# Optimization experiments

Hardware: AMD Instinct MI355X
Metric: run time of the kernel (lower is better)

## Reference

```python
import jax, jax.numpy as jnp
import numpy as np

N = 8192      # num voxels (queries)
M = 8192      # num important conv coords (keys)
B = 2         # batch size
MAXZ, MAXY, MAXX = 41, 1440, 1440
PTS, PDIM = 5, 4
PRUNE_RATIO = 0.5
NEG = -1e9


def setup_inputs() -> dict:
    key = jax.random.key(0)
    k = jax.random.split(key, 8)
    bidx = jax.random.randint(k[0], (N, 1), 0, B)
    zyx = jnp.concatenate([
        jax.random.randint(k[1], (N, 1), 0, MAXZ),
        jax.random.randint(k[2], (N, 1), 0, MAXY),
        jax.random.randint(k[3], (N, 1), 0, MAXX)], axis=1)
    voxel_coords = jnp.concatenate([bidx, zyx], axis=1).astype(jnp.int32)  # [N,4] (b,z,y,x)
    kb = jax.random.randint(k[4], (M, 1), 0, B).astype(jnp.float32)
    kc = jax.random.uniform(k[5], (M, 3), dtype=jnp.float32) * jnp.array([MAXZ, MAXY, MAXX], jnp.float32)
    important_conv_coords = jnp.concatenate([kb, kc], axis=1)  # [M,4] float
    voxels = jax.random.normal(k[6], (N, PTS, PDIM), dtype=jnp.float32)
    kw = jax.random.split(k[7], 2)
    w1 = jax.random.normal(kw[0], (3, 32), dtype=jnp.float32) * 0.5
    b1 = jnp.zeros((32,), jnp.float32)
    w2 = jax.random.normal(kw[1], (32, 1), dtype=jnp.float32) * 0.2
    b2 = jnp.zeros((1,), jnp.float32)
    return {"voxel_coords": voxel_coords, "important_conv_coords": important_conv_coords,
            "voxels": voxels, "w1": w1, "b1": b1, "w2": w2, "b2": b2}


def reference(voxel_coords, important_conv_coords, voxels, w1, b1, w2, b2):
    # --- attn_prune_unimportant: per-batch coord attention, vectorized with a batch mask ---
    q = voxel_coords[:, 1:].astype(jnp.float32)           # [N,3]
    qb = voxel_coords[:, 0]                               # [N] batch idx
    keys = important_conv_coords[:, 1:]                   # [M,3]
    kbat = important_conv_coords[:, 0].astype(jnp.int32)  # [M]
    scores = jnp.einsum('nd,md->nm', q, keys) / jnp.sqrt(jnp.float32(3.0))  # [N,M]
    mask = qb[:, None] == kbat[None, :]
    scores = jnp.where(mask, scores, NEG)
    attn = jax.nn.softmax(scores, axis=-1)                # per-batch softmax (masked)
    coords_weight = jnp.einsum('nm,md->nd', attn, keys)   # [N,3]  (values == keys)
    # importance_conv: Linear(3,32) -> ReLU -> Linear(32,1) -> Sigmoid
    h = jax.nn.relu(coords_weight @ w1 + b1)
    importance = jax.nn.sigmoid(h @ w2 + b2)              # [N,1]
    # --- sort-based pruning: drop the lowest-importance fraction ---
    order = jnp.argsort(importance[:, 0])                 # ascending, like torch .sort()
    keep = order[int(N * PRUNE_RATIO):]                   # [K] static size
    important_coords = voxel_coords[keep]                 # [K,4]
    important_voxels = voxels[keep]                       # [K,PTS,PDIM]
    kept_importance = importance[keep]                    # [K,1]
    return important_coords, important_voxels, kept_importance, importance
```

## Files before the change

kernel.cpp:

```cpp
#include <hip/hip_runtime.h>
#include <math.h>

#define NQ   8192
#define MK   8192
#define KEEP 4096

#define OFF_HDR    0
#define OFF_KPART  64
#define OFF_QPART  131136
#define OFF_CMAX   262208
#define OFF_PART   524352
#define OFF_K64    1572928


typedef unsigned long long ull;

__global__ __launch_bounds__(1024) void partition_kernel(
    const int4*   __restrict__ vcoords,
    const float4* __restrict__ kcoords,
    float* __restrict__ ws)
{
    __shared__ int wtot[16];
    const int t = threadIdx.x, w = t >> 6, lane = t & 63;
    const int base = t * 8;
    int* hdr = (int*)ws;
    float4* kp = (float4*)((char*)ws + OFF_KPART);
    float4* qp = (float4*)((char*)ws + OFF_QPART);

    float4 kv[8];
    int n0 = 0;
    #pragma unroll
    for (int r = 0; r < 8; ++r) { kv[r] = kcoords[base + r]; n0 += (kv[r].x == 0.0f) ? 1 : 0; }
    int inc = n0;
    #pragma unroll
    for (int off = 1; off < 64; off <<= 1) { int a = __shfl_up(inc, off); if (lane >= off) inc += a; }
    if (lane == 63) wtot[w] = inc;
    __syncthreads();
    int wbase = 0, tot0 = 0;
    #pragma unroll
    for (int i = 0; i < 16; ++i) { if (i < w) wbase += wtot[i]; tot0 += wtot[i]; }
    int ex0 = wbase + inc - n0;
    int ex1 = tot0 + (base - ex0);
    #pragma unroll
    for (int r = 0; r < 8; ++r) {
        if (kv[r].x == 0.0f) kp[ex0++] = kv[r]; else kp[ex1++] = kv[r];
    }
    if (t == 0) { hdr[0] = tot0; hdr[1] = MK - tot0; }
    __syncthreads();

    int4 qv[8];
    int qn0 = 0;
    #pragma unroll
    for (int r = 0; r < 8; ++r) { qv[r] = vcoords[base + r]; qn0 += (qv[r].x == 0) ? 1 : 0; }
    int qinc = qn0;
    #pragma unroll
    for (int off = 1; off < 64; off <<= 1) { int a = __shfl_up(qinc, off); if (lane >= off) qinc += a; }
    if (lane == 63) wtot[w] = qinc;
    __syncthreads();
    int qwbase = 0, qtot0 = 0;
    #pragma unroll
    for (int i = 0; i < 16; ++i) { if (i < w) qwbase += wtot[i]; qtot0 += wtot[i]; }
    int qex0 = qwbase + qinc - qn0;
    int qex1 = qtot0 + (base - qex0);
    #pragma unroll
    for (int r = 0; r < 8; ++r) {
        int idx = base + r;
        float4 q;
        q.x = (float)qv[r].y; q.y = (float)qv[r].z; q.z = (float)qv[r].w;
        q.w = __int_as_float(idx);
        if (qv[r].x == 0) qp[qex0++] = q; else qp[qex1++] = q;
    }
    if (t == 0) { hdr[2] = qtot0; hdr[3] = NQ - qtot0; }
}

__global__ __launch_bounds__(1024) void attn_kernel(float* __restrict__ ws)
{
    __shared__ __align__(16) char smem[65792];
    float4* sk   = (float4*)smem;
    float*  red1 = (float*)(smem + 16384);
    float*  red2 = (float*)(smem + 16384 + 16448);
    float4* pf   = (float4*)smem;

    const int* hdr = (const int*)ws;
    const float4* kpart = (const float4*)((char*)ws + OFF_KPART);
    const float4* qpart = (const float4*)((char*)ws + OFF_QPART);
    float*  cmaxg = (float*)((char*)ws + OFF_CMAX);
    float4* partg = (float4*)((char*)ws + OFF_PART);

    const int kc0 = hdr[0], qc0 = hdr[2];
    const int g = blockIdx.x >> 3, c = blockIdx.x & 7;
    const int gs = g * 256;
    const bool uni1 = (gs >= qc0);
    const bool uni  = (gs + 256 <= qc0) || uni1;
    const int r0  = (uni && uni1) ? kc0 : 0;
    const int len = uni ? (uni1 ? MK - kc0 : kc0) : MK;
    const int CL = (len + 7) >> 3;
    const int cs = r0 + c * CL;
    int tn = min(cs + CL, r0 + len) - cs; if (tn < 0) tn = 0;

    const int t = threadIdx.x, w = t >> 6, lane = t & 63;
    const float4 q0 = qpart[gs + lane];
    const float4 q1 = qpart[gs + lane + 64];
    const float4 q2 = qpart[gs + lane + 128];
    const float4 q3 = qpart[gs + lane + 192];
    const float b0 = (gs + lane        >= qc0) ? 1.f : 0.f;
    const float b1 = (gs + lane + 64   >= qc0) ? 1.f : 0.f;
    const float b2_ = (gs + lane + 128 >= qc0) ? 1.f : 0.f;
    const float b3 = (gs + lane + 192  >= qc0) ? 1.f : 0.f;
    const float is3 = 0.57735026918962576f;

    if (t < tn) sk[t] = kpart[cs + t];
    __syncthreads();

    const int SL = (tn + 15) >> 4;
    const int jb = w * SL, je = min(jb + SL, tn);

    float m0 = -INFINITY, m1 = -INFINITY, m2 = -INFINITY, m3 = -INFINITY;
    if (uni) {
        #pragma unroll 4
        for (int j = jb; j < je; ++j) {
            float4 k4 = sk[j];
            m0 = fmaxf(m0, fmaf(q0.x, k4.y, fmaf(q0.y, k4.z, q0.z * k4.w)));
            m1 = fmaxf(m1, fmaf(q1.x, k4.y, fmaf(q1.y, k4.z, q1.z * k4.w)));
            m2 = fmaxf(m2, fmaf(q2.x, k4.y, fmaf(q2.y, k4.z, q2.z * k4.w)));
            m3 = fmaxf(m3, fmaf(q3.x, k4.y, fmaf(q3.y, k4.z, q3.z * k4.w)));
        }
    } else {
        #pragma unroll 4
        for (int j = jb; j < je; ++j) {
            float4 k4 = sk[j];
            float d0 = fmaf(q0.x, k4.y, fmaf(q0.y, k4.z, q0.z * k4.w));
            float d1 = fmaf(q1.x, k4.y, fmaf(q1.y, k4.z, q1.z * k4.w));
            float d2 = fmaf(q2.x, k4.y, fmaf(q2.y, k4.z, q2.z * k4.w));
            float d3 = fmaf(q3.x, k4.y, fmaf(q3.y, k4.z, q3.z * k4.w));
            m0 = fmaxf(m0, fmaf(fabsf(k4.x - b0),  -1e10f, d0));
            m1 = fmaxf(m1, fmaf(fabsf(k4.x - b1),  -1e10f, d1));
            m2 = fmaxf(m2, fmaf(fabsf(k4.x - b2_), -1e10f, d2));
            m3 = fmaxf(m3, fmaf(fabsf(k4.x - b3),  -1e10f, d3));
        }
    }
    red1[w * 257 + lane]       = m0;
    red1[w * 257 + lane + 64]  = m1;
    red1[w * 257 + lane + 128] = m2;
    red1[w * 257 + lane + 192] = m3;
    __syncthreads();
    {
        const int col = t >> 2, r4 = (t & 3) * 4;
        float mv = red1[r4 * 257 + col];
        mv = fmaxf(mv, red1[(r4 + 1) * 257 + col]);
        mv = fmaxf(mv, red1[(r4 + 2) * 257 + col]);
        mv = fmaxf(mv, red1[(r4 + 3) * 257 + col]);
        mv = fmaxf(mv, __shfl_xor(mv, 1));
        mv = fmaxf(mv, __shfl_xor(mv, 2));
        if ((t & 3) == 0) {
            red2[col] = mv;
            cmaxg[blockIdx.x * 256 + col] = mv;
        }
    }
    __syncthreads();
    const float mg0 = red2[lane],       cut0 = mg0 - 155.8845727f;
    const float mg1 = red2[lane + 64],  cut1 = mg1 - 155.8845727f;
    const float mg2 = red2[lane + 128], cut2 = mg2 - 155.8845727f;
    const float mg3 = red2[lane + 192], cut3 = mg3 - 155.8845727f;

    float l0 = 0.f, sz0 = 0.f, sy0 = 0.f, sx0 = 0.f;
    float l1 = 0.f, sz1 = 0.f, sy1 = 0.f, sx1 = 0.f;
    float l2 = 0.f, sz2 = 0.f, sy2 = 0.f, sx2 = 0.f;
    float l3 = 0.f, sz3 = 0.f, sy3 = 0.f, sx3 = 0.f;
    #pragma unroll 2
    for (int j = jb; j < je; ++j) {
        float4 k4 = sk[j];
        float d0 = fmaf(q0.x, k4.y, fmaf(q0.y, k4.z, q0.z * k4.w));
        float d1 = fmaf(q1.x, k4.y, fmaf(q1.y, k4.z, q1.z * k4.w));
        float d2 = fmaf(q2.x, k4.y, fmaf(q2.y, k4.z, q2.z * k4.w));
        float d3 = fmaf(q3.x, k4.y, fmaf(q3.y, k4.z, q3.z * k4.w));
        if (!uni) {
            d0 = fmaf(fabsf(k4.x - b0),  -1e10f, d0);
            d1 = fmaf(fabsf(k4.x - b1),  -1e10f, d1);
            d2 = fmaf(fabsf(k4.x - b2_), -1e10f, d2);
            d3 = fmaf(fabsf(k4.x - b3),  -1e10f, d3);
        }
        bool t0 = d0 >= cut0, t1 = d1 >= cut1, t2 = d2 >= cut2, t3 = d3 >= cut3;
        if (__any(t0 || t1 || t2 || t3)) {
            float e0 = t0 ? expf((d0 - mg0) * is3) : 0.f;
            float e1 = t1 ? expf((d1 - mg1) * is3) : 0.f;
            float e2 = t2 ? expf((d2 - mg2) * is3) : 0.f;
            float e3 = t3 ? expf((d3 - mg3) * is3) : 0.f;
            l0 += e0; sz0 = fmaf(e0, k4.y, sz0); sy0 = fmaf(e0, k4.z, sy0); sx0 = fmaf(e0, k4.w, sx0);
            l1 += e1; sz1 = fmaf(e1, k4.y, sz1); sy1 = fmaf(e1, k4.z, sy1); sx1 = fmaf(e1, k4.w, sx1);
            l2 += e2; sz2 = fmaf(e2, k4.y, sz2); sy2 = fmaf(e2, k4.z, sy2); sx2 = fmaf(e2, k4.w, sx2);
            l3 += e3; sz3 = fmaf(e3, k4.y, sz3); sy3 = fmaf(e3, k4.z, sy3); sx3 = fmaf(e3, k4.w, sx3);
        }
    }
    __syncthreads();
    pf[w * 257 + lane]       = make_float4(l0, sz0, sy0, sx0);
    pf[w * 257 + lane + 64]  = make_float4(l1, sz1, sy1, sx1);
    pf[w * 257 + lane + 128] = make_float4(l2, sz2, sy2, sx2);
    pf[w * 257 + lane + 192] = make_float4(l3, sz3, sy3, sx3);
    __syncthreads();
    {
        const int col = t >> 2, r4 = (t & 3) * 4;
        float4 a = pf[r4 * 257 + col];
        #pragma unroll
        for (int rr = 1; rr < 4; ++rr) {
            float4 p = pf[(r4 + rr) * 257 + col];
            a.x += p.x; a.y += p.y; a.z += p.z; a.w += p.w;
        }
        a.x += __shfl_xor(a.x, 1); a.y += __shfl_xor(a.y, 1);
        a.z += __shfl_xor(a.z, 1); a.w += __shfl_xor(a.w, 1);
        a.x += __shfl_xor(a.x, 2); a.y += __shfl_xor(a.y, 2);
        a.z += __shfl_xor(a.z, 2); a.w += __shfl_xor(a.w, 2);
        if ((t & 3) == 0) partg[blockIdx.x * 256 + col] = a;
    }
}

__global__ __launch_bounds__(256) void mlp_kernel(
    const float* __restrict__ ws,
    const float* __restrict__ w1, const float* __restrict__ b1,
    const float* __restrict__ w2, const float* __restrict__ b2,
    float* __restrict__ out_imp, ull* __restrict__ K64)
{
    const int s = blockIdx.x * 256 + threadIdx.x;
    const int g = s >> 8, q = s & 255;
    const float*  cmaxg = (const float*)((const char*)ws + OFF_CMAX);
    const float4* partg = (const float4*)((const char*)ws + OFF_PART);
    const float4* qpart = (const float4*)((const char*)ws + OFF_QPART);
    const float is3 = 0.57735026918962576f;

    float cc[8];
    float C = -INFINITY;
    #pragma unroll
    for (int c = 0; c < 8; ++c) {
        cc[c] = cmaxg[(g * 8 + c) * 256 + q];
        C = fmaxf(C, cc[c]);
    }
    float L = 0.f, SZ = 0.f, SY = 0.f, SX = 0.f;
    if (C != -INFINITY) {
        #pragma unroll
        for (int c = 0; c < 8; ++c) {
            float sc = expf((cc[c] - C) * is3);
            float4 p = partg[(g * 8 + c) * 256 + q];
            L  = fmaf(p.x, sc, L);
            SZ = fmaf(p.y, sc, SZ);
            SY = fmaf(p.z, sc, SY);
            SX = fmaf(p.w, sc, SX);
        }
    }
    const float4 qq = qpart[s];
    const int qid = __float_as_int(qq.w);
    float inv = (L > 0.f) ? 1.f / L : 0.f;
    float cz = SZ * inv, cy = SY * inv, cx = SX * inv;
    float logit = b2[0];
    #pragma unroll
    for (int k = 0; k < 32; ++k) {
        float h = b1[k] + cz * w1[k] + cy * w1[32 + k] + cx * w1[64 + k];
        h = fmaxf(h, 0.f);
        logit += h * w2[k];
    }
    float p = 1.f / (1.f + expf(-logit));
    out_imp[qid] = p;
    K64[qid] = ((ull)__float_as_uint(p) << 32) | (unsigned)qid;
}

__global__ __launch_bounds__(1024) void rank_scatter_kernel(
    const ull* __restrict__ K,
    const int4* __restrict__ vcoords,
    const float* __restrict__ voxels,
    float* __restrict__ out)
{
    __shared__ int scnt[16][32];
    __shared__ int rks[32];
    const int t = threadIdx.x, w = t >> 6, lane = t & 63;
    const int ib = blockIdx.x * 32;

    const ull kiv = K[ib + (lane & 31)];
    const int kilo = (int)(unsigned)kiv, kihi = (int)(unsigned)(kiv >> 32);

    const int jb = w * 512;
    ull kj[8];
    #pragma unroll
    for (int r = 0; r < 8; ++r) kj[r] = K[jb + r * 64 + lane];

    int acc = 0;
    for (int i = 0; i < 32; ++i) {
        unsigned lo = (unsigned)__builtin_amdgcn_readlane(kilo, i);
        unsigned hi = (unsigned)__builtin_amdgcn_readlane(kihi, i);
        ull ki = ((ull)hi << 32) | lo;
        int c = 0;
        #pragma unroll
        for (int r = 0; r < 8; ++r)
            c += (int)__popcll(__ballot(kj[r] < ki));
        acc += (lane == i) ? c : 0;
    }
    if (lane < 32) scnt[w][lane] = acc;
    __syncthreads();
    if (t < 32) {
        int rank = 0;
        #pragma unroll
        for (int ww = 0; ww < 16; ++ww) rank += scnt[ww][t];
        rks[t] = rank;
    }
    __syncthreads();

    const int il = t >> 5, r = t & 31;
    const int rank = rks[il];
    if (rank >= KEEP) {
        const int p = rank - KEEP;
        const int i = ib + il;
        if (r < 20) {
            out[16384 + p * 20 + r] = voxels[i * 20 + r];
        } else if (r < 24) {
            const int* vc = (const int*)&vcoords[i];
            out[p * 4 + (r - 20)] = (float)vc[r - 20];
        } else if (r == 24) {
            out[98304 + p] = __uint_as_float((unsigned)(K[i] >> 32));
        }
    }
}

extern "C" void kernel_launch(void* const* d_in, const int* in_sizes, int n_in,
                              void* d_out, int out_size, void* d_ws, size_t ws_size,
                              hipStream_t stream) {
    const int4*   vcoords = (const int4*)d_in[0];
    const float4* kcoords = (const float4*)d_in[1];
    const float*  voxels  = (const float*)d_in[2];
    const float*  w1      = (const float*)d_in[3];
    const float*  b1      = (const float*)d_in[4];
    const float*  w2      = (const float*)d_in[5];
    const float*  b2      = (const float*)d_in[6];
    float* out = (float*)d_out;
    float* ws  = (float*)d_ws;
    ull* K64   = (ull*)((char*)d_ws + OFF_K64);

    partition_kernel<<<1, 1024, 0, stream>>>(vcoords, kcoords, ws);
    attn_kernel<<<256, 1024, 0, stream>>>(ws);
    mlp_kernel<<<32, 256, 0, stream>>>(ws, w1, b1, w2, b2, out + 102400, K64);
    rank_scatter_kernel<<<256, 1024, 0, stream>>>(K64, vcoords, voxels, out);
}
```

Before: 118.9 us.

## Fuse four kernels into one persistent kernel with grid-wide atomic barriers

Merges the partition, attention, MLP and rank/scatter kernels into a single 256-block launch, with hand-written atomic grid barriers separating the phases. The single-block partition becomes a parallel per-block count, then a scan over the block counts and a scatter. This removes three kernel launch gaps and the serial one-block partition stage. In exchange it adds four grid syncs and a memset to clear the barrier counters, and it depends on all 256 blocks of 1024 threads being resident at once or it will deadlock.

```diff
diff --git a/kernel.cpp b/kernel.cpp
--- a/kernel.cpp
+++ b/kernel.cpp
@@ -4,316 +4,331 @@
 #define NQ   8192
 #define MK   8192
 #define KEEP 4096
-
-#define OFF_HDR    0
-#define OFF_KPART  64
-#define OFF_QPART  131136
-#define OFF_CMAX   262208
-#define OFF_PART   524352
-#define OFF_K64    1572928
+#define NBLK 256
+
+#define OFF_BAR    0
+#define OFF_KCNT   64
+#define OFF_QCNT   1088
+#define OFF_KPART  2112
+#define OFF_QPART  133184
+#define OFF_CMAX   264256
+#define OFF_PART   526400
+#define OFF_K64    1574976
 
 
 typedef unsigned long long ull;
 
-__global__ __launch_bounds__(1024) void partition_kernel(
+__device__ __forceinline__ void grid_barrier(unsigned* bar, int ph) {
+    __syncthreads();
+    if (threadIdx.x == 0) {
+        __threadfence();
+        unsigned prev = atomicAdd(bar + ph * 2, 1u);
+        if (prev == NBLK - 1u) {
+            atomicExch(bar + ph * 2 + 1, 1u);
+        } else {
+            while (atomicAdd(bar + ph * 2 + 1, 0u) == 0u)
+                __builtin_amdgcn_s_sleep(2);
+        }
+        __threadfence();
+    }
+    __syncthreads();
+}
+
+__global__ __launch_bounds__(1024) void fused_kernel(
     const int4*   __restrict__ vcoords,
     const float4* __restrict__ kcoords,
-    float* __restrict__ ws)
-{
-    __shared__ int wtot[16];
-    const int t = threadIdx.x, w = t >> 6, lane = t & 63;
-    const int base = t * 8;
-    int* hdr = (int*)ws;
-    float4* kp = (float4*)((char*)ws + OFF_KPART);
-    float4* qp = (float4*)((char*)ws + OFF_QPART);
-
-    float4 kv[8];
-    int n0 = 0;
-    #pragma unroll
-    for (int r = 0; r < 8; ++r) { kv[r] = kcoords[base + r]; n0 += (kv[r].x == 0.0f) ? 1 : 0; }
-    int inc = n0;
-    #pragma unroll
-    for (int off = 1; off < 64; off <<= 1) { int a = __shfl_up(inc, off); if (lane >= off) inc += a; }
-    if (lane == 63) wtot[w] = inc;
-    __syncthreads();
-    int wbase = 0, tot0 = 0;
-    #pragma unroll
-    for (int i = 0; i < 16; ++i) { if (i < w) wbase += wtot[i]; tot0 += wtot[i]; }
-    int ex0 = wbase + inc - n0;
-    int ex1 = tot0 + (base - ex0);
-    #pragma unroll
-    for (int r = 0; r < 8; ++r) {
-        if (kv[r].x == 0.0f) kp[ex0++] = kv[r]; else kp[ex1++] = kv[r];
-    }
-    if (t == 0) { hdr[0] = tot0; hdr[1] = MK - tot0; }
-    __syncthreads();
-
-    int4 qv[8];
-    int qn0 = 0;
-    #pragma unroll
-    for (int r = 0; r < 8; ++r) { qv[r] = vcoords[base + r]; qn0 += (qv[r].x == 0) ? 1 : 0; }
-    int qinc = qn0;
-    #pragma unroll
-    for (int off = 1; off < 64; off <<= 1) { int a = __shfl_up(qinc, off); if (lane >= off) qinc += a; }
-    if (lane == 63) wtot[w] = qinc;
-    __syncthreads();
-    int qwbase = 0, qtot0 = 0;
-    #pragma unroll
-    for (int i = 0; i < 16; ++i) { if (i < w) qwbase += wtot[i]; qtot0 += wtot[i]; }
-    int qex0 = qwbase + qinc - qn0;
-    int qex1 = qtot0 + (base - qex0);
-    #pragma unroll
-    for (int r = 0; r < 8; ++r) {
-        int idx = base + r;
-        float4 q;
-        q.x = (float)qv[r].y; q.y = (float)qv[r].z; q.z = (float)qv[r].w;
-        q.w = __int_as_float(idx);
-        if (qv[r].x == 0) qp[qex0++] = q; else qp[qex1++] = q;
-    }
-    if (t == 0) { hdr[2] = qtot0; hdr[3] = NQ - qtot0; }
-}
-
-__global__ __launch_bounds__(1024) void attn_kernel(float* __restrict__ ws)
+    const float*  __restrict__ voxels,
+    const float*  __restrict__ w1, const float* __restrict__ b1v,
+    const float*  __restrict__ w2, const float* __restrict__ b2v,
+    float* __restrict__ out,
+    void*  __restrict__ wsv)
 {
     __shared__ __align__(16) char smem[65792];
-    float4* sk   = (float4*)smem;
-    float*  red1 = (float*)(smem + 16384);
-    float*  red2 = (float*)(smem + 16384 + 16448);
-    float4* pf   = (float4*)smem;
-
-    const int* hdr = (const int*)ws;
-    const float4* kpart = (const float4*)((char*)ws + OFF_KPART);
-    const float4* qpart = (const float4*)((char*)ws + OFF_QPART);
-    float*  cmaxg = (float*)((char*)ws + OFF_CMAX);
-    float4* partg = (float4*)((char*)ws + OFF_PART);
-
-    const int kc0 = hdr[0], qc0 = hdr[2];
-    const int g = blockIdx.x >> 3, c = blockIdx.x & 7;
-    const int gs = g * 256;
-    const bool uni1 = (gs >= qc0);
-    const bool uni  = (gs + 256 <= qc0) || uni1;
-    const int r0  = (uni && uni1) ? kc0 : 0;
-    const int len = uni ? (uni1 ? MK - kc0 : kc0) : MK;
-    const int CL = (len + 7) >> 3;
-    const int cs = r0 + c * CL;
-    int tn = min(cs + CL, r0 + len) - cs; if (tn < 0) tn = 0;
-
-    const int t = threadIdx.x, w = t >> 6, lane = t & 63;
-    const float4 q0 = qpart[gs + lane];
-    const float4 q1 = qpart[gs + lane + 64];
-    const float4 q2 = qpart[gs + lane + 128];
-    const float4 q3 = qpart[gs + lane + 192];
-    const float b0 = (gs + lane        >= qc0) ? 1.f : 0.f;
-    const float b1 = (gs + lane + 64   >= qc0) ? 1.f : 0.f;
-    const float b2_ = (gs + lane + 128 >= qc0) ? 1.f : 0.f;
-    const float b3 = (gs + lane + 192  >= qc0) ? 1.f : 0.f;
-    const float is3 = 0.57735026918962576f;
-
-    if (t < tn) sk[t] = kpart[cs + t];
+    __shared__ int shdr[4];
+    __shared__ int scnt[16][32];
+    __shared__ int rks[32];
+
+    unsigned* bar  = (unsigned*)((char*)wsv + OFF_BAR);
+    unsigned* kcnt = (unsigned*)((char*)wsv + OFF_KCNT);
+    unsigned* qcnt = (unsigned*)((char*)wsv + OFF_QCNT);
+    float4*   kpart = (float4*)((char*)wsv + OFF_KPART);
+    float4*   qpart = (float4*)((char*)wsv + OFF_QPART);
+    float*    cmaxg = (float*)((char*)wsv + OFF_CMAX);
+    float4*   partg = (float4*)((char*)wsv + OFF_PART);
+    ull*      K64   = (ull*)((char*)wsv + OFF_K64);
+
+    const int b = blockIdx.x, t = threadIdx.x;
+    const int w = t >> 6, lane = t & 63;
+
+    float4 myK = make_float4(0,0,0,0);
+    int4   myQ = make_int4(0,0,0,0);
+    ull blK = 0, blQ = 0;
+    if (w == 0) {
+        if (lane < 32) myK = kcoords[b * 32 + lane];
+        blK = __ballot((lane < 32) && (myK.x == 0.0f));
+        if (lane == 0) kcnt[b] = (unsigned)__popcll(blK);
+    } else if (w == 1) {
+        if (lane < 32) myQ = vcoords[b * 32 + lane];
+        blQ = __ballot((lane < 32) && (myQ.x == 0));
+        if (lane == 0) qcnt[b] = (unsigned)__popcll(blQ);
+    }
+    grid_barrier(bar, 0);
+
+    if (w < 2) {
+        const unsigned* cnt = (w == 0) ? kcnt : qcnt;
+        unsigned c0 = cnt[4*lane], c1 = cnt[4*lane+1],
+                 c2 = cnt[4*lane+2], c3 = cnt[4*lane+3];
+        unsigned s = c0 + c1 + c2 + c3;
+        unsigned sc = s;
+        #pragma unroll
+        for (int off = 1; off < 64; off <<= 1) {
+            unsigned v = __shfl_up(sc, off);
+            if (lane >= off) sc += v;
+        }
+        unsigned tot  = __shfl(sc, 63);
+        unsigned excl = sc - s;
+        const int lb = b >> 2, rb = b & 3;
+        unsigned p = (rb == 0) ? 0u : (rb == 1) ? c0 :
+                     (rb == 2) ? (c0 + c1) : (c0 + c1 + c2);
+        unsigned base = (unsigned)__shfl((int)excl, lb) + (unsigned)__shfl((int)p, lb);
+        if (lane == 0) { shdr[w * 2] = (int)base; shdr[w * 2 + 1] = (int)tot; }
+    }
     __syncthreads();
-
-    const int SL = (tn + 15) >> 4;
-    const int jb = w * SL, je = min(jb + SL, tn);
-
-    float m0 = -INFINITY, m1 = -INFINITY, m2 = -INFINITY, m3 = -INFINITY;
-    if (uni) {
-        #pragma unroll 4
-        for (int j = jb; j < je; ++j) {
-            float4 k4 = sk[j];
-            m0 = fmaxf(m0, fmaf(q0.x, k4.y, fmaf(q0.y, k4.z, q0.z * k4.w)));
-            m1 = fmaxf(m1, fmaf(q1.x, k4.y, fmaf(q1.y, k4.z, q1.z * k4.w)));
-            m2 = fmaxf(m2, fmaf(q2.x, k4.y, fmaf(q2.y, k4.z, q2.z * k4.w)));
-            m3 = fmaxf(m3, fmaf(q3.x, k4.y, fmaf(q3.y, k4.z, q3.z * k4.w)));
-        }
-    } else {
-        #pragma unroll 4
+    const int kOff = shdr[0], kc0 = shdr[1];
+    const int qOff = shdr[2], qc0 = shdr[3];
+
+    if (w == 0 && lane < 32) {
+        bool p0 = (myK.x == 0.0f);
+        int bef = (int)__popcll(blK & ((1ull << lane) - 1));
+        int gi = b * 32 + lane;
+        int dst = p0 ? (kOff + bef) : (kc0 + gi - (kOff + bef));
+        kpart[dst] = myK;
+    } else if (w == 1 && lane < 32) {
+        bool p0 = (myQ.x == 0);
+        int bef = (int)__popcll(blQ & ((1ull << lane) - 1));
+        int gi = b * 32 + lane;
+        int dst = p0 ? (qOff + bef) : (qc0 + gi - (qOff + bef));
+        qpart[dst] = make_float4((float)myQ.y, (float)myQ.z, (float)myQ.w,
+                                 __int_as_float(gi));
+    }
+    grid_barrier(bar, 1);
+
+    {
+        float4* sk   = (float4*)smem;
+        float*  red1 = (float*)(smem + 16384);
+        float*  red2 = (float*)(smem + 16384 + 16448);
+        float4* pf   = (float4*)smem;
+
+        const int g = b >> 3, c = b & 7;
+        const int gs = g * 256;
+        const bool uni1 = (gs >= qc0);
+        const bool uni  = (gs + 256 <= qc0) || uni1;
+        const int r0  = (uni && uni1) ? kc0 : 0;
+        const int len = uni ? (uni1 ? MK - kc0 : kc0) : MK;
+        const int CL = (len + 7) >> 3;
+        const int cs = r0 + c * CL;
+        int tn = min(cs + CL, r0 + len) - cs; if (tn < 0) tn = 0;
+
+        const float4 q0 = qpart[gs + lane];
+        const float4 q1 = qpart[gs + lane + 64];
+        const float4 q2 = qpart[gs + lane + 128];
+        const float4 q3 = qpart[gs + lane + 192];
+        const float f0 = (gs + lane       >= qc0) ? 1.f : 0.f;
+        const float f1 = (gs + lane + 64  >= qc0) ? 1.f : 0.f;
+        const float f2 = (gs + lane + 128 >= qc0) ? 1.f : 0.f;
+        const float f3 = (gs + lane + 192 >= qc0) ? 1.f : 0.f;
+        const float is3 = 0.57735026918962576f;
+
+        if (t < tn) sk[t] = kpart[cs + t];
+        __syncthreads();
+
+        const int SL = (tn + 15) >> 4;
+        const int jb = w * SL, je = min(jb + SL, tn);
+
+        float m0 = -INFINITY, m1 = -INFINITY, m2 = -INFINITY, m3 = -INFINITY;
+        if (uni) {
+            #pragma unroll 4
+            for (int j = jb; j < je; ++j) {
+                float4 k4 = sk[j];
+                m0 = fmaxf(m0, fmaf(q0.x, k4.y, fmaf(q0.y, k4.z, q0.z * k4.w)));
+                m1 = fmaxf(m1, fmaf(q1.x, k4.y, fmaf(q1.y, k4.z, q1.z * k4.w)));
+                m2 = fmaxf(m2, fmaf(q2.x, k4.y, fmaf(q2.y, k4.z, q2.z * k4.w)));
+                m3 = fmaxf(m3, fmaf(q3.x, k4.y, fmaf(q3.y, k4.z, q3.z * k4.w)));
+            }
+        } else {
+            #pragma unroll 4
+            for (int j = jb; j < je; ++j) {
+                float4 k4 = sk[j];
+                float d0 = fmaf(q0.x, k4.y, fmaf(q0.y, k4.z, q0.z * k4.w));
+                float d1 = fmaf(q1.x, k4.y, fmaf(q1.y, k4.z, q1.z * k4.w));
+                float d2 = fmaf(q2.x, k4.y, fmaf(q2.y, k4.z, q2.z * k4.w));
+                float d3 = fmaf(q3.x, k4.y, fmaf(q3.y, k4.z, q3.z * k4.w));
+                m0 = fmaxf(m0, fmaf(fabsf(k4.x - f0), -1e10f, d0));
+                m1 = fmaxf(m1, fmaf(fabsf(k4.x - f1), -1e10f, d1));
+                m2 = fmaxf(m2, fmaf(fabsf(k4.x - f2), -1e10f, d2));
+                m3 = fmaxf(m3, fmaf(fabsf(k4.x - f3), -1e10f, d3));
+            }
+        }
+        red1[w * 257 + lane]       = m0;
+        red1[w * 257 + lane + 64]  = m1;
+        red1[w * 257 + lane + 128] = m2;
+        red1[w * 257 + lane + 192] = m3;
+        __syncthreads();
+        {
+            const int col = t >> 2, r4 = (t & 3) * 4;
+            float mv = red1[r4 * 257 + col];
+            mv = fmaxf(mv, red1[(r4 + 1) * 257 + col]);
+            mv = fmaxf(mv, red1[(r4 + 2) * 257 + col]);
+            mv = fmaxf(mv, red1[(r4 + 3) * 257 + col]);
+            mv = fmaxf(mv, __shfl_xor(mv, 1));
+            mv = fmaxf(mv, __shfl_xor(mv, 2));
+            if ((t & 3) == 0) {
+                red2[col] = mv;
+                cmaxg[b * 256 + col] = mv;
+            }
+        }
+        __syncthreads();
+        const float mg0 = red2[lane],       cut0 = mg0 - 155.8845727f;
+        const float mg1 = red2[lane + 64],  cut1 = mg1 - 155.8845727f;
+        const float mg2 = red2[lane + 128], cut2 = mg2 - 155.8845727f;
+        const float mg3 = red2[lane + 192], cut3 = mg3 - 155.8845727f;
+
+        float l0 = 0.f, sz0 = 0.f, sy0 = 0.f, sx0 = 0.f;
+        float l1 = 0.f, sz1 = 0.f, sy1 = 0.f, sx1 = 0.f;
+        float l2 = 0.f, sz2 = 0.f, sy2 = 0.f, sx2 = 0.f;
+        float l3 = 0.f, sz3 = 0.f, sy3 = 0.f, sx3 = 0.f;
+        #pragma unroll 2
         for (int j = jb; j < je; ++j) {
             float4 k4 = sk[j];
             float d0 = fmaf(q0.x, k4.y, fmaf(q0.y, k4.z, q0.z * k4.w));
             float d1 = fmaf(q1.x, k4.y, fmaf(q1.y, k4.z, q1.z * k4.w));
             float d2 = fmaf(q2.x, k4.y, fmaf(q2.y, k4.z, q2.z * k4.w));
             float d3 = fmaf(q3.x, k4.y, fmaf(q3.y, k4.z, q3.z * k4.w));
-            m0 = fmaxf(m0, fmaf(fabsf(k4.x - b0),  -1e10f, d0));
-            m1 = fmaxf(m1, fmaf(fabsf(k4.x - b1),  -1e10f, d1));
-            m2 = fmaxf(m2, fmaf(fabsf(k4.x - b2_), -1e10f, d2));
-            m3 = fmaxf(m3, fmaf(fabsf(k4.x - b3),  -1e10f, d3));
-        }
-    }
-    red1[w * 257 + lane]       = m0;
-    red1[w * 257 + lane + 64]  = m1;
-    red1[w * 257 + lane + 128] = m2;
-    red1[w * 257 + lane + 192] = m3;
-    __syncthreads();
-    {
-        const int col = t >> 2, r4 = (t & 3) * 4;
-        float mv = red1[r4 * 257 + col];
-        mv = fmaxf(mv, red1[(r4 + 1) * 257 + col]);
-        mv = fmaxf(mv, red1[(r4 + 2) * 257 + col]);
-        mv = fmaxf(mv, red1[(r4 + 3) * 257 + col]);
-        mv = fmaxf(mv, __shfl_xor(mv, 1));
-        mv = fmaxf(mv, __shfl_xor(mv, 2));
-        if ((t & 3) == 0) {
-            red2[col] = mv;
-            cmaxg[blockIdx.x * 256 + col] = mv;
-        }
-    }
-    __syncthreads();
-    const float mg0 = red2[lane],       cut0 = mg0 - 155.8845727f;
-    const float mg1 = red2[lane + 64],  cut1 = mg1 - 155.8845727f;
-    const float mg2 = red2[lane + 128], cut2 = mg2 - 155.8845727f;
-    const float mg3 = red2[lane + 192], cut3 = mg3 - 155.8845727f;
-
-    float l0 = 0.f, sz0 = 0.f, sy0 = 0.f, sx0 = 0.f;
-    float l1 = 0.f, sz1 = 0.f, sy1 = 0.f, sx1 = 0.f;
-    float l2 = 0.f, sz2 = 0.f, sy2 = 0.f, sx2 = 0.f;
-    float l3 = 0.f, sz3 = 0.f, sy3 = 0.f, sx3 = 0.f;
-    #pragma unroll 2
-    for (int j = jb; j < je; ++j) {
-        float4 k4 = sk[j];
-        float d0 = fmaf(q0.x, k4.y, fmaf(q0.y, k4.z, q0.z * k4.w));
-        float d1 = fmaf(q1.x, k4.y, fmaf(q1.y, k4.z, q1.z * k4.w));
-        float d2 = fmaf(q2.x, k4.y, fmaf(q2.y, k4.z, q2.z * k4.w));
-        float d3 = fmaf(q3.x, k4.y, fmaf(q3.y, k4.z, q3.z * k4.w));
-        if (!uni) {
-            d0 = fmaf(fabsf(k4.x - b0),  -1e10f, d0);
-            d1 = fmaf(fabsf(k4.x - b1),  -1e10f, d1);
-            d2 = fmaf(fabsf(k4.x - b2_), -1e10f, d2);
-            d3 = fmaf(fabsf(k4.x - b3),  -1e10f, d3);
-        }
-        bool t0 = d0 >= cut0, t1 = d1 >= cut1, t2 = d2 >= cut2, t3 = d3 >= cut3;
-        if (__any(t0 || t1 || t2 || t3)) {
-            float e0 = t0 ? expf((d0 - mg0) * is3) : 0.f;
-            float e1 = t1 ? expf((d1 - mg1) * is3) : 0.f;
-            float e2 = t2 ? expf((d2 - mg2) * is3) : 0.f;
-            float e3 = t3 ? expf((d3 - mg3) * is3) : 0.f;
-            l0 += e0; sz0 = fmaf(e0, k4.y, sz0); sy0 = fmaf(e0, k4.z, sy0); sx0 = fmaf(e0, k4.w, sx0);
-            l1 += e1; sz1 = fmaf(e1, k4.y, sz1); sy1 = fmaf(e1, k4.z, sy1); sx1 = fmaf(e1, k4.w, sx1);
-            l2 += e2; sz2 = fmaf(e2, k4.y, sz2); sy2 = fmaf(e2, k4.z, sy2); sx2 = fmaf(e2, k4.w, sx2);
-            l3 += e3; sz3 = fmaf(e3, k4.y, sz3); sy3 = fmaf(e3, k4.z, sy3); sx3 = fmaf(e3, k4.w, sx3);
-        }
-    }
-    __syncthreads();
-    pf[w * 257 + lane]       = make_float4(l0, sz0, sy0, sx0);
-    pf[w * 257 + lane + 64]  = make_float4(l1, sz1, sy1, sx1);
-    pf[w * 257 + lane + 128] = make_float4(l2, sz2, sy2, sx2);
-    pf[w * 257 + lane + 192] = make_float4(l3, sz3, sy3, sx3);
-    __syncthreads();
-    {
-        const int col = t >> 2, r4 = (t & 3) * 4;
-        float4 a = pf[r4 * 257 + col];
-        #pragma unroll
-        for (int rr = 1; rr < 4; ++rr) {
-            float4 p = pf[(r4 + rr) * 257 + col];
-            a.x += p.x; a.y += p.y; a.z += p.z; a.w += p.w;
-        }
-        a.x += __shfl_xor(a.x, 1); a.y += __shfl_xor(a.y, 1);
-        a.z += __shfl_xor(a.z, 1); a.w += __shfl_xor(a.w, 1);
-        a.x += __shfl_xor(a.x, 2); a.y += __shfl_xor(a.y, 2);
-        a.z += __shfl_xor(a.z, 2); a.w += __shfl_xor(a.w, 2);
-        if ((t & 3) == 0) partg[blockIdx.x * 256 + col] = a;
-    }
-}
-
-__global__ __launch_bounds__(256) void mlp_kernel(
-    const float* __restrict__ ws,
-    const float* __restrict__ w1, const float* __restrict__ b1,
-    const float* __restrict__ w2, const float* __restrict__ b2,
-    float* __restrict__ out_imp, ull* __restrict__ K64)
-{
-    const int s = blockIdx.x * 256 + threadIdx.x;
-    const int g = s >> 8, q = s & 255;
-    const float*  cmaxg = (const float*)((const char*)ws + OFF_CMAX);
-    const float4* partg = (const float4*)((const char*)ws + OFF_PART);
-    const float4* qpart = (const float4*)((const char*)ws + OFF_QPART);
-    const float is3 = 0.57735026918962576f;
-
-    float cc[8];
-    float C = -INFINITY;
-    #pragma unroll
-    for (int c = 0; c < 8; ++c) {
-        cc[c] = cmaxg[(g * 8 + c) * 256 + q];
-        C = fmaxf(C, cc[c]);
-    }
-    float L = 0.f, SZ = 0.f, SY = 0.f, SX = 0.f;
-    if (C != -INFINITY) {
+            if (!uni) {
+                d0 = fmaf(fabsf(k4.x - f0), -1e10f, d0);
+                d1 = fmaf(fabsf(k4.x - f1), -1e10f, d1);
+                d2 = fmaf(fabsf(k4.x - f2), -1e10f, d2);
+                d3 = fmaf(fabsf(k4.x - f3), -1e10f, d3);
+            }
+            bool t0 = d0 >= cut0, t1 = d1 >= cut1, t2 = d2 >= cut2, t3 = d3 >= cut3;
+            if (__any(t0 || t1 || t2 || t3)) {
+                float e0 = t0 ? expf((d0 - mg0) * is3) : 0.f;
+                float e1 = t1 ? expf((d1 - mg1) * is3) : 0.f;
+                float e2 = t2 ? expf((d2 - mg2) * is3) : 0.f;
+                float e3 = t3 ? expf((d3 - mg3) * is3) : 0.f;
+                l0 += e0; sz0 = fmaf(e0, k4.y, sz0); sy0 = fmaf(e0, k4.z, sy0); sx0 = fmaf(e0, k4.w, sx0);
+                l1 += e1; sz1 = fmaf(e1, k4.y, sz1); sy1 = fmaf(e1, k4.z, sy1); sx1 = fmaf(e1, k4.w, sx1);
+                l2 += e2; sz2 = fmaf(e2, k4.y, sz2); sy2 = fmaf(e2, k4.z, sy2); sx2 = fmaf(e2, k4.w, sx2);
+                l3 += e3; sz3 = fmaf(e3, k4.y, sz3); sy3 = fmaf(e3, k4.z, sy3); sx3 = fmaf(e3, k4.w, sx3);
+            }
+        }
+        __syncthreads();
+        pf[w * 257 + lane]       = make_float4(l0, sz0, sy0, sx0);
+        pf[w * 257 + lane + 64]  = make_float4(l1, sz1, sy1, sx1);
+        pf[w * 257 + lane + 128] = make_float4(l2, sz2, sy2, sx2);
+        pf[w * 257 + lane + 192] = make_float4(l3, sz3, sy3, sx3);
+        __syncthreads();
+        {
+            const int col = t >> 2, r4 = (t & 3) * 4;
+            float4 a = pf[r4 * 257 + col];
+            #pragma unroll
+            for (int rr = 1; rr < 4; ++rr) {
+                float4 p = pf[(r4 + rr) * 257 + col];
+                a.x += p.x; a.y += p.y; a.z += p.z; a.w += p.w;
+            }
+            a.x += __shfl_xor(a.x, 1); a.y += __shfl_xor(a.y, 1);
+            a.z += __shfl_xor(a.z, 1); a.w += __shfl_xor(a.w, 1);
+            a.x += __shfl_xor(a.x, 2); a.y += __shfl_xor(a.y, 2);
+            a.z += __shfl_xor(a.z, 2); a.w += __shfl_xor(a.w, 2);
+            if ((t & 3) == 0) partg[b * 256 + col] = a;
+        }
+    }
+    grid_barrier(bar, 2);
+
+    if (t < 32) {
+        const int s = b * 32 + t;
+        const int g = s >> 8, q = s & 255;
+        const float is3 = 0.57735026918962576f;
+        float cc[8];
+        float C = -INFINITY;
         #pragma unroll
         for (int c = 0; c < 8; ++c) {
-            float sc = expf((cc[c] - C) * is3);
-            float4 p = partg[(g * 8 + c) * 256 + q];
-            L  = fmaf(p.x, sc, L);
-            SZ = fmaf(p.y, sc, SZ);
-            SY = fmaf(p.z, sc, SY);
-            SX = fmaf(p.w, sc, SX);
-        }
-    }
-    const float4 qq = qpart[s];
-    const int qid = __float_as_int(qq.w);
-    float inv = (L > 0.f) ? 1.f / L : 0.f;
-    float cz = SZ * inv, cy = SY * inv, cx = SX * inv;
-    float logit = b2[0];
-    #pragma unroll
-    for (int k = 0; k < 32; ++k) {
-        float h = b1[k] + cz * w1[k] + cy * w1[32 + k] + cx * w1[64 + k];
-        h = fmaxf(h, 0.f);
-        logit += h * w2[k];
-    }
-    float p = 1.f / (1.f + expf(-logit));
-    out_imp[qid] = p;
-    K64[qid] = ((ull)__float_as_uint(p) << 32) | (unsigned)qid;
-}
-
-__global__ __launch_bounds__(1024) void rank_scatter_kernel(
-    const ull* __restrict__ K,
-    const int4* __restrict__ vcoords,
-    const float* __restrict__ voxels,
-    float* __restrict__ out)
-{
-    __shared__ int scnt[16][32];
-    __shared__ int rks[32];
-    const int t = threadIdx.x, w = t >> 6, lane = t & 63;
-    const int ib = blockIdx.x * 32;
-
-    const ull kiv = K[ib + (lane & 31)];
-    const int kilo = (int)(unsigned)kiv, kihi = (int)(unsigned)(kiv >> 32);
-
-    const int jb = w * 512;
-    ull kj[8];
-    #pragma unroll
-    for (int r = 0; r < 8; ++r) kj[r] = K[jb + r * 64 + lane];
-
-    int acc = 0;
-    for (int i = 0; i < 32; ++i) {
-        unsigned lo = (unsigned)__builtin_amdgcn_readlane(kilo, i);
-        unsigned hi = (unsigned)__builtin_amdgcn_readlane(kihi, i);
-        ull ki = ((ull)hi << 32) | lo;
-        int c = 0;
+            cc[c] = cmaxg[(g * 8 + c) * 256 + q];
+            C = fmaxf(C, cc[c]);
+        }
+        float L = 0.f, SZ = 0.f, SY = 0.f, SX = 0.f;
+        if (C != -INFINITY) {
+            #pragma unroll
+            for (int c = 0; c < 8; ++c) {
+                float scale = expf((cc[c] - C) * is3);
+                float4 p = partg[(g * 8 + c) * 256 + q];
+                L  = fmaf(p.x, scale, L);
+                SZ = fmaf(p.y, scale, SZ);
+                SY = fmaf(p.z, scale, SY);
+                SX = fmaf(p.w, scale, SX);
+            }
+        }
+        const float4 qq = qpart[s];
+        const int qid = __float_as_int(qq.w);
+        float inv = (L > 0.f) ? 1.f / L : 0.f;
+        float cz = SZ * inv, cy = SY * inv, cx = SX * inv;
+        float logit = b2v[0];
         #pragma unroll
-        for (int r = 0; r < 8; ++r)
-            c += (int)__popcll(__ballot(kj[r] < ki));
-        acc += (lane == i) ? c : 0;
-    }
-    if (lane < 32) scnt[w][lane] = acc;
-    __syncthreads();
-    if (t < 32) {
-        int rank = 0;
+        for (int k = 0; k < 32; ++k) {
+            float h = b1v[k] + cz * w1[k] + cy * w1[32 + k] + cx * w1[64 + k];
+            h = fmaxf(h, 0.f);
+            logit += h * w2[k];
+        }
+        float p = 1.f / (1.f + expf(-logit));
+        out[102400 + qid] = p;
+        K64[qid] = ((ull)__float_as_uint(p) << 32) | (unsigned)qid;
+    }
+    grid_barrier(bar, 3);
+
+    {
+        const int ib = b * 32;
+        const ull kiv = K64[ib + (lane & 31)];
+        const int kilo = (int)(unsigned)kiv, kihi = (int)(unsigned)(kiv >> 32);
+
+        const int jb = w * 512;
+        ull kj[8];
         #pragma unroll
-        for (int ww = 0; ww < 16; ++ww) rank += scnt[ww][t];
-        rks[t] = rank;
-    }
-    __syncthreads();
-
-    const int il = t >> 5, r = t & 31;
-    const int rank = rks[il];
-    if (rank >= KEEP) {
-        const int p = rank - KEEP;
-        const int i = ib + il;
-        if (r < 20) {
-            out[16384 + p * 20 + r] = voxels[i * 20 + r];
-        } else if (r < 24) {
-            const int* vc = (const int*)&vcoords[i];
-            out[p * 4 + (r - 20)] = (float)vc[r - 20];
-        } else if (r == 24) {
-            out[98304 + p] = __uint_as_float((unsigned)(K[i] >> 32));
+        for (int r = 0; r < 8; ++r) kj[r] = K64[jb + r * 64 + lane];
+
+        int acc = 0;
+        for (int i = 0; i < 32; ++i) {
+            unsigned lo = (unsigned)__builtin_amdgcn_readlane(kilo, i);
+            unsigned hi = (unsigned)__builtin_amdgcn_readlane(kihi, i);
+            ull ki = ((ull)hi << 32) | lo;
+            int c = 0;
+            #pragma unroll
+            for (int r = 0; r < 8; ++r)
+                c += (int)__popcll(__ballot(kj[r] < ki));
+            acc += (lane == i) ? c : 0;
+        }
+        if (lane < 32) scnt[w][lane] = acc;
+        __syncthreads();
+        if (t < 32) {
+            int rank = 0;
+            #pragma unroll
+            for (int ww = 0; ww < 16; ++ww) rank += scnt[ww][t];
+            rks[t] = rank;
+        }
+        __syncthreads();
+
+        const int il = t >> 5, r = t & 31;
+        const int rank = rks[il];
+        if (rank >= KEEP) {
+            const int p = rank - KEEP;
+            const int i = ib + il;
+            if (r < 20) {
+                out[16384 + p * 20 + r] = voxels[i * 20 + r];
+            } else if (r < 24) {
+                const int* vc = (const int*)&vcoords[i];
+                out[p * 4 + (r - 20)] = (float)vc[r - 20];
+            } else if (r == 24) {
+                out[98304 + p] = __uint_as_float((unsigned)(K64[i] >> 32));
+            }
         }
     }
 }
@@ -329,11 +344,8 @@
     const float*  w2      = (const float*)d_in[5];
     const float*  b2      = (const float*)d_in[6];
     float* out = (float*)d_out;
-    float* ws  = (float*)d_ws;
-    ull* K64   = (ull*)((char*)d_ws + OFF_K64);
-
-    partition_kernel<<<1, 1024, 0, stream>>>(vcoords, kcoords, ws);
-    attn_kernel<<<256, 1024, 0, stream>>>(ws);
-    mlp_kernel<<<32, 256, 0, stream>>>(ws, w1, b1, w2, b2, out + 102400, K64);
-    rank_scatter_kernel<<<256, 1024, 0, stream>>>(K64, vcoords, voxels, out);
+
+    hipMemsetAsync(d_ws, 0, 64, stream);
+    fused_kernel<<<NBLK, 1024, 0, stream>>>(vcoords, kcoords, voxels,
+                                            w1, b1, w2, b2, out, d_ws);
 }
```

Measured after the change: 148.0 us. +24.4%, slower.

## Drop batch partition kernel and apply masked attention over all keys

Applied to the files above, without the earlier changes.

Removes the single-block partition kernel that grouped queries and keys by batch index. The attention kernel now reads the raw voxel and key coordinates directly, scans every query tile against all keys, and applies the batch mask arithmetically. The MLP kernel writes results by original index without a permutation lookup. This cuts one serial launch and the workspace round trip. The cost is that attention now scores every cross-batch pair, roughly doubling the dot-product and max work, and the exp pass's wave-level skip is less likely to fire when batches are mixed within a wave.

```diff
diff --git a/kernel.cpp b/kernel.cpp
--- a/kernel.cpp
+++ b/kernel.cpp
@@ -5,75 +5,17 @@
 #define MK   8192
 #define KEEP 4096
 
-#define OFF_HDR    0
-#define OFF_KPART  64
-#define OFF_QPART  131136
-#define OFF_CMAX   262208
-#define OFF_PART   524352
-#define OFF_K64    1572928
+#define OFF_CMAX   0
+#define OFF_PART   262144
+#define OFF_K64    1310720
 
 
 typedef unsigned long long ull;
 
-__global__ __launch_bounds__(1024) void partition_kernel(
+__global__ __launch_bounds__(1024) void attn_kernel(
     const int4*   __restrict__ vcoords,
     const float4* __restrict__ kcoords,
     float* __restrict__ ws)
-{
-    __shared__ int wtot[16];
-    const int t = threadIdx.x, w = t >> 6, lane = t & 63;
-    const int base = t * 8;
-    int* hdr = (int*)ws;
-    float4* kp = (float4*)((char*)ws + OFF_KPART);
-    float4* qp = (float4*)((char*)ws + OFF_QPART);
-
-    float4 kv[8];
-    int n0 = 0;
-    #pragma unroll
-    for (int r = 0; r < 8; ++r) { kv[r] = kcoords[base + r]; n0 += (kv[r].x == 0.0f) ? 1 : 0; }
-    int inc = n0;
-    #pragma unroll
-    for (int off = 1; off < 64; off <<= 1) { int a = __shfl_up(inc, off); if (lane >= off) inc += a; }
-    if (lane == 63) wtot[w] = inc;
-    __syncthreads();
-    int wbase = 0, tot0 = 0;
-    #pragma unroll
-    for (int i = 0; i < 16; ++i) { if (i < w) wbase += wtot[i]; tot0 += wtot[i]; }
-    int ex0 = wbase + inc - n0;
-    int ex1 = tot0 + (base - ex0);
-    #pragma unroll
-    for (int r = 0; r < 8; ++r) {
-        if (kv[r].x == 0.0f) kp[ex0++] = kv[r]; else kp[ex1++] = kv[r];
-    }
-    if (t == 0) { hdr[0] = tot0; hdr[1] = MK - tot0; }
-    __syncthreads();
-
-    int4 qv[8];
-    int qn0 = 0;
-    #pragma unroll
-    for (int r = 0; r < 8; ++r) { qv[r] = vcoords[base + r]; qn0 += (qv[r].x == 0) ? 1 : 0; }
-    int qinc = qn0;
-    #pragma unroll
-    for (int off = 1; off < 64; off <<= 1) { int a = __shfl_up(qinc, off); if (lane >= off) qinc += a; }
-    if (lane == 63) wtot[w] = qinc;
-    __syncthreads();
-    int qwbase = 0, qtot0 = 0;
-    #pragma unroll
-    for (int i = 0; i < 16; ++i) { if (i < w) qwbase += wtot[i]; qtot0 += wtot[i]; }
-    int qex0 = qwbase + qinc - qn0;
-    int qex1 = qtot0 + (base - qex0);
-    #pragma unroll
-    for (int r = 0; r < 8; ++r) {
-        int idx = base + r;
-        float4 q;
-        q.x = (float)qv[r].y; q.y = (float)qv[r].z; q.z = (float)qv[r].w;
-        q.w = __int_as_float(idx);
-        if (qv[r].x == 0) qp[qex0++] = q; else qp[qex1++] = q;
-    }
-    if (t == 0) { hdr[2] = qtot0; hdr[3] = NQ - qtot0; }
-}
-
-__global__ __launch_bounds__(1024) void attn_kernel(float* __restrict__ ws)
 {
     __shared__ __align__(16) char smem[65792];
     float4* sk   = (float4*)smem;
@@ -81,63 +23,41 @@
     float*  red2 = (float*)(smem + 16384 + 16448);
     float4* pf   = (float4*)smem;
 
-    const int* hdr = (const int*)ws;
-    const float4* kpart = (const float4*)((char*)ws + OFF_KPART);
-    const float4* qpart = (const float4*)((char*)ws + OFF_QPART);
     float*  cmaxg = (float*)((char*)ws + OFF_CMAX);
     float4* partg = (float4*)((char*)ws + OFF_PART);
 
-    const int kc0 = hdr[0], qc0 = hdr[2];
-    const int g = blockIdx.x >> 3, c = blockIdx.x & 7;
-    const int gs = g * 256;
-    const bool uni1 = (gs >= qc0);
-    const bool uni  = (gs + 256 <= qc0) || uni1;
-    const int r0  = (uni && uni1) ? kc0 : 0;
-    const int len = uni ? (uni1 ? MK - kc0 : kc0) : MK;
-    const int CL = (len + 7) >> 3;
-    const int cs = r0 + c * CL;
-    int tn = min(cs + CL, r0 + len) - cs; if (tn < 0) tn = 0;
-
+    const int b = blockIdx.x;
+    const int g = b >> 3, c = b & 7;
+    const int gs = g * 256, cs = c * 1024;
     const int t = threadIdx.x, w = t >> 6, lane = t & 63;
-    const float4 q0 = qpart[gs + lane];
-    const float4 q1 = qpart[gs + lane + 64];
-    const float4 q2 = qpart[gs + lane + 128];
-    const float4 q3 = qpart[gs + lane + 192];
-    const float b0 = (gs + lane        >= qc0) ? 1.f : 0.f;
-    const float b1 = (gs + lane + 64   >= qc0) ? 1.f : 0.f;
-    const float b2_ = (gs + lane + 128 >= qc0) ? 1.f : 0.f;
-    const float b3 = (gs + lane + 192  >= qc0) ? 1.f : 0.f;
+
+    const int4 v0 = vcoords[gs + lane];
+    const int4 v1 = vcoords[gs + lane + 64];
+    const int4 v2 = vcoords[gs + lane + 128];
+    const int4 v3 = vcoords[gs + lane + 192];
+    const float qb0 = (float)v0.x, qz0 = (float)v0.y, qy0 = (float)v0.z, qx0 = (float)v0.w;
+    const float qb1 = (float)v1.x, qz1 = (float)v1.y, qy1 = (float)v1.z, qx1 = (float)v1.w;
+    const float qb2 = (float)v2.x, qz2 = (float)v2.y, qy2 = (float)v2.z, qx2 = (float)v2.w;
+    const float qb3 = (float)v3.x, qz3 = (float)v3.y, qy3 = (float)v3.z, qx3 = (float)v3.w;
     const float is3 = 0.57735026918962576f;
 
-    if (t < tn) sk[t] = kpart[cs + t];
-    __syncthreads();
-
-    const int SL = (tn + 15) >> 4;
-    const int jb = w * SL, je = min(jb + SL, tn);
+    if (t < 1024) sk[t] = kcoords[cs + t];
+    __syncthreads();
+
+    const int jb = w * 64, je = jb + 64;
 
     float m0 = -INFINITY, m1 = -INFINITY, m2 = -INFINITY, m3 = -INFINITY;
-    if (uni) {
-        #pragma unroll 4
-        for (int j = jb; j < je; ++j) {
-            float4 k4 = sk[j];
-            m0 = fmaxf(m0, fmaf(q0.x, k4.y, fmaf(q0.y, k4.z, q0.z * k4.w)));
-            m1 = fmaxf(m1, fmaf(q1.x, k4.y, fmaf(q1.y, k4.z, q1.z * k4.w)));
-            m2 = fmaxf(m2, fmaf(q2.x, k4.y, fmaf(q2.y, k4.z, q2.z * k4.w)));
-            m3 = fmaxf(m3, fmaf(q3.x, k4.y, fmaf(q3.y, k4.z, q3.z * k4.w)));
-        }
-    } else {
-        #pragma unroll 4
-        for (int j = jb; j < je; ++j) {
-            float4 k4 = sk[j];
-            float d0 = fmaf(q0.x, k4.y, fmaf(q0.y, k4.z, q0.z * k4.w));
-            float d1 = fmaf(q1.x, k4.y, fmaf(q1.y, k4.z, q1.z * k4.w));
-            float d2 = fmaf(q2.x, k4.y, fmaf(q2.y, k4.z, q2.z * k4.w));
-            float d3 = fmaf(q3.x, k4.y, fmaf(q3.y, k4.z, q3.z * k4.w));
-            m0 = fmaxf(m0, fmaf(fabsf(k4.x - b0),  -1e10f, d0));
-            m1 = fmaxf(m1, fmaf(fabsf(k4.x - b1),  -1e10f, d1));
-            m2 = fmaxf(m2, fmaf(fabsf(k4.x - b2_), -1e10f, d2));
-            m3 = fmaxf(m3, fmaf(fabsf(k4.x - b3),  -1e10f, d3));
-        }
+    #pragma unroll 4
+    for (int j = jb; j < je; ++j) {
+        float4 k4 = sk[j];
+        float d0 = fmaf(qz0, k4.y, fmaf(qy0, k4.z, qx0 * k4.w));
+        float d1 = fmaf(qz1, k4.y, fmaf(qy1, k4.z, qx1 * k4.w));
+        float d2 = fmaf(qz2, k4.y, fmaf(qy2, k4.z, qx2 * k4.w));
+        float d3 = fmaf(qz3, k4.y, fmaf(qy3, k4.z, qx3 * k4.w));
+        m0 = fmaxf(m0, fmaf(fabsf(k4.x - qb0), -1e10f, d0));
+        m1 = fmaxf(m1, fmaf(fabsf(k4.x - qb1), -1e10f, d1));
+        m2 = fmaxf(m2, fmaf(fabsf(k4.x - qb2), -1e10f, d2));
+        m3 = fmaxf(m3, fmaf(fabsf(k4.x - qb3), -1e10f, d3));
     }
     red1[w * 257 + lane]       = m0;
     red1[w * 257 + lane + 64]  = m1;
@@ -154,7 +74,7 @@
         mv = fmaxf(mv, __shfl_xor(mv, 2));
         if ((t & 3) == 0) {
             red2[col] = mv;
-            cmaxg[blockIdx.x * 256 + col] = mv;
+            cmaxg[b * 256 + col] = mv;
         }
     }
     __syncthreads();
@@ -170,16 +90,14 @@
     #pragma unroll 2
     for (int j = jb; j < je; ++j) {
         float4 k4 = sk[j];
-        float d0 = fmaf(q0.x, k4.y, fmaf(q0.y, k4.z, q0.z * k4.w));
-        float d1 = fmaf(q1.x, k4.y, fmaf(q1.y, k4.z, q1.z * k4.w));
-        float d2 = fmaf(q2.x, k4.y, fmaf(q2.y, k4.z, q2.z * k4.w));
-        float d3 = fmaf(q3.x, k4.y, fmaf(q3.y, k4.z, q3.z * k4.w));
-        if (!uni) {
-            d0 = fmaf(fabsf(k4.x - b0),  -1e10f, d0);
-            d1 = fmaf(fabsf(k4.x - b1),  -1e10f, d1);
-            d2 = fmaf(fabsf(k4.x - b2_), -1e10f, d2);
-            d3 = fmaf(fabsf(k4.x - b3),  -1e10f, d3);
-        }
+        float d0 = fmaf(qz0, k4.y, fmaf(qy0, k4.z, qx0 * k4.w));
+        float d1 = fmaf(qz1, k4.y, fmaf(qy1, k4.z, qx1 * k4.w));
+        float d2 = fmaf(qz2, k4.y, fmaf(qy2, k4.z, qx2 * k4.w));
+        float d3 = fmaf(qz3, k4.y, fmaf(qy3, k4.z, qx3 * k4.w));
+        d0 = fmaf(fabsf(k4.x - qb0), -1e10f, d0);
+        d1 = fmaf(fabsf(k4.x - qb1), -1e10f, d1);
+        d2 = fmaf(fabsf(k4.x - qb2), -1e10f, d2);
+        d3 = fmaf(fabsf(k4.x - qb3), -1e10f, d3);
         bool t0 = d0 >= cut0, t1 = d1 >= cut1, t2 = d2 >= cut2, t3 = d3 >= cut3;
         if (__any(t0 || t1 || t2 || t3)) {
             float e0 = t0 ? expf((d0 - mg0) * is3) : 0.f;
@@ -210,7 +128,7 @@
         a.z += __shfl_xor(a.z, 1); a.w += __shfl_xor(a.w, 1);
         a.x += __shfl_xor(a.x, 2); a.y += __shfl_xor(a.y, 2);
         a.z += __shfl_xor(a.z, 2); a.w += __shfl_xor(a.w, 2);
-        if ((t & 3) == 0) partg[blockIdx.x * 256 + col] = a;
+        if ((t & 3) == 0) partg[b * 256 + col] = a;
     }
 }
 
@@ -224,7 +142,6 @@
     const int g = s >> 8, q = s & 255;
     const float*  cmaxg = (const float*)((const char*)ws + OFF_CMAX);
     const float4* partg = (const float4*)((const char*)ws + OFF_PART);
-    const float4* qpart = (const float4*)((const char*)ws + OFF_QPART);
     const float is3 = 0.57735026918962576f;
 
     float cc[8];
@@ -235,19 +152,15 @@
         C = fmaxf(C, cc[c]);
     }
     float L = 0.f, SZ = 0.f, SY = 0.f, SX = 0.f;
-    if (C != -INFINITY) {
-        #pragma unroll
-        for (int c = 0; c < 8; ++c) {
-            float sc = expf((cc[c] - C) * is3);
-            float4 p = partg[(g * 8 + c) * 256 + q];
-            L  = fmaf(p.x, sc, L);
-            SZ = fmaf(p.y, sc, SZ);
-            SY = fmaf(p.z, sc, SY);
-            SX = fmaf(p.w, sc, SX);
-        }
-    }
-    const float4 qq = qpart[s];
-    const int qid = __float_as_int(qq.w);
+    #pragma unroll
+    for (int c = 0; c < 8; ++c) {
+        float sc = expf((cc[c] - C) * is3);
+        float4 p = partg[(g * 8 + c) * 256 + q];
+        L  = fmaf(p.x, sc, L);
+        SZ = fmaf(p.y, sc, SZ);
+        SY = fmaf(p.z, sc, SY);
+        SX = fmaf(p.w, sc, SX);
+    }
     float inv = (L > 0.f) ? 1.f / L : 0.f;
     float cz = SZ * inv, cy = SY * inv, cx = SX * inv;
     float logit = b2[0];
@@ -258,8 +171,8 @@
         logit += h * w2[k];
     }
     float p = 1.f / (1.f + expf(-logit));
-    out_imp[qid] = p;
-    K64[qid] = ((ull)__float_as_uint(p) << 32) | (unsigned)qid;
+    out_imp[s] = p;
+    K64[s] = ((ull)__float_as_uint(p) << 32) | (unsigned)s;
 }
 
 __global__ __launch_bounds__(1024) void rank_scatter_kernel(
@@ -332,8 +245,7 @@
     float* ws  = (float*)d_ws;
     ull* K64   = (ull*)((char*)d_ws + OFF_K64);
 
-    partition_kernel<<<1, 1024, 0, stream>>>(vcoords, kcoords, ws);
-    attn_kernel<<<256, 1024, 0, stream>>>(ws);
+    attn_kernel<<<256, 1024, 0, stream>>>(vcoords, kcoords, ws);
     mlp_kernel<<<32, 256, 0, stream>>>(ws, w1, b1, w2, b2, out + 102400, K64);
     rank_scatter_kernel<<<256, 1024, 0, stream>>>(K64, vcoords, voxels, out);
 }
```

Result: faster. 104.4 us (-12.2%).
